# Optimization experiments

Hardware: AMD Instinct MI355X
Metric: run time of the kernel (lower is better)

Reference implementation:

```python
import jax, jax.numpy as jnp
import numpy as np

B, S, D = 4, 2048, 384
H, KVH, HD = 6, 2, 64
GROUPS = H // KVH  # 3
ROPE_THETA = 100000.0


def _rope_tables(seq_len, head_dim, theta):
    inv = 1.0 / (theta ** (np.arange(0, head_dim, 2, dtype=np.float32) / head_dim))
    t = np.arange(seq_len, dtype=np.float32)
    freqs = np.outer(t, inv)  # [S, HD//2]
    return jnp.asarray(np.cos(freqs)), jnp.asarray(np.sin(freqs))


def setup_inputs() -> dict:
    key = jax.random.key(0)
    ks = jax.random.split(key, 5)
    hidden_states = jax.random.normal(ks[0], (B, S, D), dtype=jnp.float32)
    Wq = jax.random.normal(ks[1], (D, H * HD), dtype=jnp.float32) * 0.02
    Wk = jax.random.normal(ks[2], (D, KVH * HD), dtype=jnp.float32) * 0.02
    Wv = jax.random.normal(ks[3], (D, KVH * HD), dtype=jnp.float32) * 0.02
    Wo = jax.random.normal(ks[4], (H * HD, D), dtype=jnp.float32) * 0.02
    freqs_cos, freqs_sin = _rope_tables(S, HD, ROPE_THETA)
    return {"hidden_states": hidden_states, "Wq": Wq, "Wk": Wk, "Wv": Wv,
            "Wo": Wo, "freqs_cos": freqs_cos, "freqs_sin": freqs_sin}


def _apply_rope(x, cos, sin):
    # x: [B, S, h, HD]; treat pairs (even, odd) as complex, multiply by e^{i theta}
    xr = x.reshape(*x.shape[:-1], HD // 2, 2)
    x0, x1 = xr[..., 0], xr[..., 1]
    c = cos[None, :, None, :]  # [1, S, 1, HD//2]
    s = sin[None, :, None, :]
    o0 = x0 * c - x1 * s
    o1 = x0 * s + x1 * c
    return jnp.stack([o0, o1], axis=-1).reshape(x.shape)


def reference(hidden_states, Wq, Wk, Wv, Wo, freqs_cos, freqs_sin):
    Bc, Sc, _ = hidden_states.shape
    q = (hidden_states @ Wq).reshape(Bc, Sc, H, HD)
    k = (hidden_states @ Wk).reshape(Bc, Sc, KVH, HD)
    v = (hidden_states @ Wv).reshape(Bc, Sc, KVH, HD)
    q = _apply_rope(q, freqs_cos, freqs_sin)
    k = _apply_rope(k, freqs_cos, freqs_sin)
    # repeat_interleave over the head dim (GQA group broadcast)
    k = jnp.repeat(k, GROUPS, axis=2)  # [B, S, H, HD]
    v = jnp.repeat(v, GROUPS, axis=2)
    scale = 1.0 / jnp.sqrt(jnp.float32(HD))
    scores = jnp.einsum('bqhd,bkhd->bhqk', q, k) * scale  # [B, H, S, S]
    attn = jax.nn.softmax(scores, axis=-1)
    out = jnp.einsum('bhqk,bkhd->bqhd', attn, v)  # [B, S, H, HD]
    out = out.reshape(Bc, Sc, H * HD)
    return out @ Wo
```

## Files before the change

kernel.cpp:

```cpp
#include <hip/hip_runtime.h>
#include <stdint.h>

#define BATCH   4
#define SEQ     2048
#define DMODEL  384
#define NHEAD   6
#define NKVH    2
#define HD      64
#define MTOK    (BATCH*SEQ)
#define NQKV    640
#define QSCALE  0.125f

typedef __bf16 bf16x8 __attribute__((ext_vector_type(8)));
typedef float  f32x16 __attribute__((ext_vector_type(16)));

__device__ inline unsigned short f2bf(float f) {
  union { float f; unsigned int u; } v; v.f = f;
  return (unsigned short)((v.u + 0x7fffu + ((v.u >> 16) & 1u)) >> 16);
}
__device__ inline float bf2f(unsigned short b) {
  union { unsigned int u; float f; } v; v.u = ((unsigned int)b) << 16;
  return v.f;
}
__device__ inline unsigned int pack2bf(float a, float b) {
  return (unsigned int)f2bf(a) | ((unsigned int)f2bf(b) << 16);
}

#define GLOAD16(gsrc, ldst) __builtin_amdgcn_global_load_lds( \
    (const __attribute__((address_space(1))) void*)(gsrc), \
    (__attribute__((address_space(3))) void*)(ldst), 16, 0, 0)

__global__ void prep_kernel(const float* __restrict__ X,
                            const float* __restrict__ Wq, const float* __restrict__ Wk,
                            const float* __restrict__ Wv, const float* __restrict__ Wo,
                            unsigned short* __restrict__ Xb,
                            unsigned short* __restrict__ WT,
                            unsigned short* __restrict__ WoT) {
  int idx = blockIdx.x * 256 + threadIdx.x;
  if (idx < (MTOK*DMODEL)/4) {
    float4 v = ((const float4*)X)[idx];
    union { unsigned short s[4]; uint2 u; } o;
    o.s[0] = f2bf(v.x); o.s[1] = f2bf(v.y); o.s[2] = f2bf(v.z); o.s[3] = f2bf(v.w);
    ((uint2*)Xb)[idx] = o.u;
  } else if (idx < (MTOK*DMODEL)/4 + NQKV*DMODEL) {
    int j = idx - (MTOK*DMODEL)/4;
    int n = j / DMODEL, k = j % DMODEL;
    float val = (n < 384) ? Wq[k*384 + n]
              : (n < 512) ? Wk[k*128 + (n-384)]
                          : Wv[k*128 + (n-512)];
    WT[j] = f2bf(val);
  } else if (idx < (MTOK*DMODEL)/4 + NQKV*DMODEL + DMODEL*DMODEL) {
    int j = idx - (MTOK*DMODEL)/4 - NQKV*DMODEL;
    int n = j / DMODEL, k = j % DMODEL;
    WoT[j] = f2bf(Wo[k*384 + n]);
  }
}

template<int NCOLS, bool OUT_BF16>
__global__ __launch_bounds__(256, 2)
void gemm_kernel(const unsigned short* __restrict__ A,
                 const unsigned short* __restrict__ BT,
                 void* __restrict__ Cout) {
  __shared__ unsigned short ldsA[128*64];
  __shared__ unsigned short ldsB[64*64];
  const int tid = threadIdx.x;
  const int wid = tid >> 6, lane = tid & 63;
  const int g = lane >> 5, l31 = lane & 31;
  const int wm = wid >> 1, wn = wid & 1;
  const int mbase = blockIdx.x * 128, nbase = blockIdx.y * 64;

  f32x16 c[2];
  #pragma unroll
  for (int i = 0; i < 2; ++i)
    #pragma unroll
    for (int r = 0; r < 16; ++r) c[i][r] = 0.f;

  for (int kt = 0; kt < DMODEL; kt += 64) {
    #pragma unroll
    for (int i = 0; i < 4; ++i) {
      int L = ((wid*4 + i) << 10) + lane*16;
      int row = L >> 7;
      int slot = (lane & 7) ^ (row & 7);
      GLOAD16(A + (mbase + row)*DMODEL + kt + slot*8, ((char*)ldsA) + L);
    }
    #pragma unroll
    for (int i = 0; i < 2; ++i) {
      int L = ((wid*2 + i) << 10) + lane*16;
      int row = L >> 7;
      int slot = (lane & 7) ^ (row & 7);
      GLOAD16(BT + (nbase + row)*DMODEL + kt + slot*8, ((char*)ldsB) + L);
    }
    __syncthreads();

    bf16x8 bf[4];
    {
      int row = wn*32 + l31;
      #pragma unroll
      for (int s = 0; s < 4; ++s) {
        int slot = ((s<<1) | g) ^ (row & 7);
        bf[s] = *(const bf16x8*)(((const char*)ldsB) + row*128 + slot*16);
      }
    }
    #pragma unroll
    for (int mt = 0; mt < 2; ++mt) {
      int row = wm*64 + mt*32 + l31;
      #pragma unroll
      for (int s = 0; s < 4; ++s) {
        int slot = ((s<<1) | g) ^ (row & 7);
        bf16x8 af = *(const bf16x8*)(((const char*)ldsA) + row*128 + slot*16);
        c[mt] = __builtin_amdgcn_mfma_f32_32x32x16_bf16(af, bf[s], c[mt], 0, 0, 0);
      }
    }
    __syncthreads();
  }

  #pragma unroll
  for (int mt = 0; mt < 2; ++mt)
    #pragma unroll
    for (int rr = 0; rr < 16; ++rr) {
      int m = mbase + wm*64 + mt*32 + (rr&3) + ((rr>>2)<<3) + (g<<2);
      int n = nbase + wn*32 + l31;
      float val = c[mt][rr];
      if (OUT_BF16) ((unsigned short*)Cout)[m*NCOLS + n] = f2bf(val);
      else          ((float*)Cout)[m*NCOLS + n] = val;
    }
}

__global__ void rope_kernel(unsigned short* __restrict__ qkv,
                            const float* __restrict__ fcos,
                            const float* __restrict__ fsin) {
  int t = blockIdx.x;
  int c = threadIdx.x;
  int s = t & (SEQ-1);
  int i = c & 31, col;
  float scale;
  if (c < 192) { int h = c >> 5;          col = h*64 + 2*i;        scale = QSCALE; }
  else         { int kvh = (c - 192) >> 5; col = 384 + kvh*64 + 2*i; scale = 1.0f; }
  unsigned int w = *(unsigned int*)(qkv + t*NQKV + col);
  float x0 = bf2f((unsigned short)(w & 0xffff));
  float x1 = bf2f((unsigned short)(w >> 16));
  float cs = fcos[s*32 + i], sn = fsin[s*32 + i];
  float o0 = (x0*cs - x1*sn) * scale;
  float o1 = (x0*sn + x1*cs) * scale;
  *(unsigned int*)(qkv + t*NQKV + col) = pack2bf(o0, o1);
}

__global__ void vtrans_kernel(const unsigned short* __restrict__ qkv,
                              unsigned short* __restrict__ VT) {
  int idx = blockIdx.x * 256 + threadIdx.x;
  int sc  = idx & 255;
  int hd  = (idx >> 8) & 63;
  int kvh = (idx >> 14) & 1;
  int b   = idx >> 15;
  union { unsigned short s[8]; uint4 v; } tmp;
  #pragma unroll
  for (int u = 0; u < 8; ++u)
    tmp.s[u] = qkv[(b*SEQ + sc*8 + u)*NQKV + 512 + kvh*64 + hd];
  *(uint4*)(VT + (((b*2 + kvh)*64 + hd) << 11) + sc*8) = tmp.v;
}

__global__ __launch_bounds__(128, 2)
void attn_kernel(const unsigned short* __restrict__ qkv,
                 const unsigned short* __restrict__ VT,
                 unsigned short* __restrict__ attnO) {
  __shared__ unsigned short ldsK[64*64];
  __shared__ unsigned short ldsV[64*64];
  const int tid = threadIdx.x;
  const int wid = tid >> 6, lane = tid & 63;
  const int g = lane >> 5, l31 = lane & 31;
  const int qt = blockIdx.x, b = blockIdx.y, h = blockIdx.z;
  const int kvh = h / 3;
  const int qrow = qt*64 + wid*32 + l31;
  const int token = b*SEQ + qrow;

  bf16x8 qf[4];
  #pragma unroll
  for (int s = 0; s < 4; ++s)
    qf[s] = *(const bf16x8*)(qkv + token*NQKV + h*64 + s*16 + g*8);

  f32x16 acc0, acc1;
  #pragma unroll
  for (int r = 0; r < 16; ++r) { acc0[r] = 0.f; acc1[r] = 0.f; }
  float m = -1e30f, l = 0.f;

  const unsigned short* Kbase = qkv + (b*SEQ)*NQKV + 384 + kvh*64;
  const unsigned short* Vbase = VT + ((b*2 + kvh)*64 << 11);

  for (int kv0 = 0; kv0 < SEQ; kv0 += 64) {
    if (wid == 0) {
      #pragma unroll
      for (int i = 0; i < 8; ++i) {
        int L = (i << 10) + lane*16;
        int row = L >> 7;
        int slot = (lane & 7) ^ (row & 7);
        GLOAD16(Kbase + (kv0 + row)*NQKV + slot*8, ((char*)ldsK) + L);
      }
    } else {
      #pragma unroll
      for (int i = 0; i < 8; ++i) {
        int L = (i << 10) + lane*16;
        int row = L >> 7;
        int slot = (lane & 7) ^ (row & 7);
        GLOAD16(Vbase + (row << 11) + kv0 + slot*8, ((char*)ldsV) + L);
      }
    }
    __syncthreads();

    f32x16 c1[2];
    #pragma unroll
    for (int kvt = 0; kvt < 2; ++kvt) {
      f32x16 cc;
      #pragma unroll
      for (int r = 0; r < 16; ++r) cc[r] = 0.f;
      int row = kvt*32 + l31;
      #pragma unroll
      for (int s = 0; s < 4; ++s) {
        int slot = ((s<<1) | g) ^ (row & 7);
        bf16x8 kf = *(const bf16x8*)(((const char*)ldsK) + row*128 + slot*16);
        cc = __builtin_amdgcn_mfma_f32_32x32x16_bf16(kf, qf[s], cc, 0, 0, 0);
      }
      c1[kvt] = cc;
    }

    float pmax = -1e30f;
    #pragma unroll
    for (int kvt = 0; kvt < 2; ++kvt)
      #pragma unroll
      for (int r = 0; r < 16; ++r) pmax = fmaxf(pmax, c1[kvt][r]);
    pmax = fmaxf(pmax, __shfl_xor(pmax, 32));
    float mnew = fmaxf(m, pmax);
    float alpha = __expf(m - mnew);
    float psum = 0.f;
    #pragma unroll
    for (int kvt = 0; kvt < 2; ++kvt)
      #pragma unroll
      for (int r = 0; r < 16; ++r) {
        float p = __expf(c1[kvt][r] - mnew);
        c1[kvt][r] = p;
        psum += p;
      }
    psum += __shfl_xor(psum, 32);
    l = l*alpha + psum;
    m = mnew;
    #pragma unroll
    for (int r = 0; r < 16; ++r) { acc0[r] *= alpha; acc1[r] *= alpha; }

    #pragma unroll
    for (int kvt = 0; kvt < 2; ++kvt) {
      #pragma unroll
      for (int sl = 0; sl < 2; ++sl) {
        int rbase = sl*8;
        unsigned int w0  = pack2bf(c1[kvt][rbase+0], c1[kvt][rbase+1]);
        unsigned int w1  = pack2bf(c1[kvt][rbase+2], c1[kvt][rbase+3]);
        unsigned int wh0 = pack2bf(c1[kvt][rbase+4], c1[kvt][rbase+5]);
        unsigned int wh1 = pack2bf(c1[kvt][rbase+6], c1[kvt][rbase+7]);
        unsigned int sx0  = __shfl_xor(w0, 32);
        unsigned int sx1  = __shfl_xor(w1, 32);
        unsigned int sxh0 = __shfl_xor(wh0, 32);
        unsigned int sxh1 = __shfl_xor(wh1, 32);
        union { bf16x8 v; unsigned int u[4]; } pf;
        pf.u[0] = g ? sxh0 : w0;
        pf.u[1] = g ? sxh1 : w1;
        pf.u[2] = g ? wh0  : sx0;
        pf.u[3] = g ? wh1  : sx1;
        int kvslice = kvt*32 + sl*16;
        #pragma unroll
        for (int dt = 0; dt < 2; ++dt) {
          int row = dt*32 + l31;
          int slot = ((kvslice >> 3) + g) ^ (row & 7);
          bf16x8 vf = *(const bf16x8*)(((const char*)ldsV) + row*128 + slot*16);
          if (dt == 0) acc0 = __builtin_amdgcn_mfma_f32_32x32x16_bf16(vf, pf.v, acc0, 0, 0, 0);
          else         acc1 = __builtin_amdgcn_mfma_f32_32x32x16_bf16(vf, pf.v, acc1, 0, 0, 0);
        }
      }
    }
    __syncthreads();
  }

  float invl = 1.0f / l;
  #pragma unroll
  for (int dt = 0; dt < 2; ++dt)
    #pragma unroll
    for (int q8 = 0; q8 < 4; ++q8) {
      union { unsigned short s[4]; uint2 u; } ov;
      #pragma unroll
      for (int j = 0; j < 4; ++j) {
        float v = (dt ? acc1[q8*4+j] : acc0[q8*4+j]) * invl;
        ov.s[j] = f2bf(v);
      }
      int d = dt*32 + q8*8 + g*4;
      *(uint2*)(attnO + token*DMODEL + h*64 + d) = ov.u;
    }
}

extern "C" void kernel_launch(void* const* d_in, const int* in_sizes, int n_in,
                              void* d_out, int out_size, void* d_ws, size_t ws_size,
                              hipStream_t stream) {
  const float* X    = (const float*)d_in[0];
  const float* Wq   = (const float*)d_in[1];
  const float* Wk   = (const float*)d_in[2];
  const float* Wv   = (const float*)d_in[3];
  const float* Wo   = (const float*)d_in[4];
  const float* fcos = (const float*)d_in[5];
  const float* fsin = (const float*)d_in[6];
  char* ws = (char*)d_ws;

  unsigned short* Xb    = (unsigned short*)(ws);
  unsigned short* QKV   = (unsigned short*)(ws + 6291456);
  unsigned short* VTb   = (unsigned short*)(ws + 16777216);
  unsigned short* attnO = (unsigned short*)(ws + 18874368);
  unsigned short* WT    = (unsigned short*)(ws + 25165824);
  unsigned short* WoT   = (unsigned short*)(ws + 25657344);

  prep_kernel<<<4608, 256, 0, stream>>>(X, Wq, Wk, Wv, Wo, Xb, WT, WoT);
  gemm_kernel<NQKV, true><<<dim3(64, 10), 256, 0, stream>>>(Xb, WT, QKV);
  rope_kernel<<<MTOK, 256, 0, stream>>>(QKV, fcos, fsin);
  vtrans_kernel<<<512, 256, 0, stream>>>(QKV, VTb);
  attn_kernel<<<dim3(32, BATCH, NHEAD), 128, 0, stream>>>(QKV, VTb, attnO);
  gemm_kernel<DMODEL, false><<<dim3(64, 6), 256, 0, stream>>>(attnO, WoT, (void*)d_out);
}
```

Before: 181.5 us.

## Split KV across waves with double-buffered staging, exp2 softmax, LDS V transpose

Restructures attention so each wave handles half of the KV sequence for 32 query rows, double-buffers its own K/V tiles via async global-to-LDS loads with vmcnt waits instead of block barriers, and merges the two partial softmax states at the end through shared memory. It also folds log2(e) into the Q scale to use raw v_exp_f32, skips the rescale when the running max barely grows, packs bf16 with a hardware convert, remaps blocks for L2 locality, and rewrites the V transpose to go through an LDS tile for coalesced access. Together these aim to remove barrier stalls and exposed load latency and to shrink softmax ALU cost. In exchange the grid has more, smaller blocks, there is a cross-wave combine step, and the lazy-rescale threshold allows unnormalized values up to 2^10.

```diff
diff --git a/kernel.cpp b/kernel.cpp
--- a/kernel.cpp
+++ b/kernel.cpp
@@ -9,7 +9,7 @@
 #define HD      64
 #define MTOK    (BATCH*SEQ)
 #define NQKV    640
-#define QSCALE  0.125f
+#define QSCALE  (0.125f * 1.4426950408889634f)
 
 typedef __bf16 bf16x8 __attribute__((ext_vector_type(8)));
 typedef float  f32x16 __attribute__((ext_vector_type(16)));
@@ -25,10 +25,23 @@
 __device__ inline unsigned int pack2bf(float a, float b) {
   return (unsigned int)f2bf(a) | ((unsigned int)f2bf(b) << 16);
 }
+__device__ inline unsigned int cvtpk(float lo, float hi) {
+  unsigned int r;
+  asm("v_cvt_pk_bf16_f32 %0, %1, %2" : "=v"(r) : "v"(lo), "v"(hi));
+  return r;
+}
+__device__ inline float exp2_fast(float x) {
+  float r;
+  asm("v_exp_f32 %0, %1" : "=v"(r) : "v"(x));
+  return r;
+}
 
 #define GLOAD16(gsrc, ldst) __builtin_amdgcn_global_load_lds( \
     (const __attribute__((address_space(1))) void*)(gsrc), \
     (__attribute__((address_space(3))) void*)(ldst), 16, 0, 0)
+
+#define WAITV8() asm volatile("s_waitcnt vmcnt(8)" ::: "memory")
+#define WAITV0() asm volatile("s_waitcnt vmcnt(0)" ::: "memory")
 
 __global__ void prep_kernel(const float* __restrict__ X,
                             const float* __restrict__ Wq, const float* __restrict__ Wk,
@@ -147,150 +160,195 @@
 
 __global__ void vtrans_kernel(const unsigned short* __restrict__ qkv,
                               unsigned short* __restrict__ VT) {
-  int idx = blockIdx.x * 256 + threadIdx.x;
-  int sc  = idx & 255;
-  int hd  = (idx >> 8) & 63;
-  int kvh = (idx >> 14) & 1;
-  int b   = idx >> 15;
-  union { unsigned short s[8]; uint4 v; } tmp;
-  #pragma unroll
-  for (int u = 0; u < 8; ++u)
-    tmp.s[u] = qkv[(b*SEQ + sc*8 + u)*NQKV + 512 + kvh*64 + hd];
-  *(uint4*)(VT + (((b*2 + kvh)*64 + hd) << 11) + sc*8) = tmp.v;
+  __shared__ unsigned short tile[64][72];
+  int t = threadIdx.x;
+  int s0 = blockIdx.x * 64;
+  int kvh = blockIdx.y;
+  int b = blockIdx.z;
+  #pragma unroll
+  for (int p = 0; p < 2; ++p) {
+    int row = (t >> 3) + p*32;
+    int c8 = t & 7;
+    uint4 v = *(const uint4*)(qkv + (size_t)(b*SEQ + s0 + row)*NQKV + 512 + kvh*64 + c8*8);
+    *(uint4*)(&tile[row][c8*8]) = v;
+  }
+  __syncthreads();
+  #pragma unroll
+  for (int p = 0; p < 2; ++p) {
+    int d = (t >> 3) + p*32;
+    int sj = t & 7;
+    union { unsigned short s[8]; uint4 v; } o;
+    #pragma unroll
+    for (int u = 0; u < 8; ++u) o.s[u] = tile[sj*8 + u][d];
+    *(uint4*)(VT + (size_t)((b*2 + kvh)*64 + d)*SEQ + s0 + sj*8) = o.v;
+  }
+}
+
+__device__ __forceinline__ void stage_tile(const unsigned short* Kbase,
+                                           const unsigned short* Vbase,
+                                           int kv0, char* kbuf, char* vbuf, int lane) {
+  #pragma unroll
+  for (int i = 0; i < 4; ++i) {
+    int L = (i << 10) + lane*16;
+    int row = L >> 7;
+    int slot = (lane & 7) ^ (row & 7);
+    GLOAD16(Kbase + (kv0 + row)*NQKV + slot*8, kbuf + L);
+  }
+  #pragma unroll
+  for (int i = 0; i < 4; ++i) {
+    int L = (i << 10) + lane*16;
+    int row = L >> 6;
+    int sl4 = (lane & 3) ^ (row & 3) ^ ((row >> 2) & 3);
+    GLOAD16(Vbase + row*SEQ + kv0 + sl4*8, vbuf + L);
+  }
 }
 
 __global__ __launch_bounds__(128, 2)
 void attn_kernel(const unsigned short* __restrict__ qkv,
                  const unsigned short* __restrict__ VT,
                  unsigned short* __restrict__ attnO) {
-  __shared__ unsigned short ldsK[64*64];
-  __shared__ unsigned short ldsV[64*64];
+  __shared__ __align__(16) char smem[32768];
   const int tid = threadIdx.x;
   const int wid = tid >> 6, lane = tid & 63;
   const int g = lane >> 5, l31 = lane & 31;
-  const int qt = blockIdx.x, b = blockIdx.y, h = blockIdx.z;
+
+  int bid = blockIdx.x;
+  int e = (bid & 7)*192 + (bid >> 3);
+  int qt = e & 63;
+  int hb = e >> 6;
+  int h = hb % 6, b = hb / 6;
   const int kvh = h / 3;
-  const int qrow = qt*64 + wid*32 + l31;
-  const int token = b*SEQ + qrow;
+  const int token = b*SEQ + qt*32 + l31;
+  const int kvbase = wid * (SEQ/2);
+
+  char* kb0 = smem + wid*16384;
+  char* vb0 = kb0 + 4096;
 
   bf16x8 qf[4];
   #pragma unroll
   for (int s = 0; s < 4; ++s)
-    qf[s] = *(const bf16x8*)(qkv + token*NQKV + h*64 + s*16 + g*8);
+    qf[s] = *(const bf16x8*)(qkv + (size_t)token*NQKV + h*64 + s*16 + g*8);
 
   f32x16 acc0, acc1;
   #pragma unroll
   for (int r = 0; r < 16; ++r) { acc0[r] = 0.f; acc1[r] = 0.f; }
   float m = -1e30f, l = 0.f;
 
-  const unsigned short* Kbase = qkv + (b*SEQ)*NQKV + 384 + kvh*64;
-  const unsigned short* Vbase = VT + ((b*2 + kvh)*64 << 11);
-
-  for (int kv0 = 0; kv0 < SEQ; kv0 += 64) {
-    if (wid == 0) {
-      #pragma unroll
-      for (int i = 0; i < 8; ++i) {
-        int L = (i << 10) + lane*16;
-        int row = L >> 7;
-        int slot = (lane & 7) ^ (row & 7);
-        GLOAD16(Kbase + (kv0 + row)*NQKV + slot*8, ((char*)ldsK) + L);
-      }
-    } else {
-      #pragma unroll
-      for (int i = 0; i < 8; ++i) {
-        int L = (i << 10) + lane*16;
-        int row = L >> 7;
-        int slot = (lane & 7) ^ (row & 7);
-        GLOAD16(Vbase + (row << 11) + kv0 + slot*8, ((char*)ldsV) + L);
-      }
-    }
-    __syncthreads();
-
-    f32x16 c1[2];
-    #pragma unroll
-    for (int kvt = 0; kvt < 2; ++kvt) {
-      f32x16 cc;
-      #pragma unroll
-      for (int r = 0; r < 16; ++r) cc[r] = 0.f;
-      int row = kvt*32 + l31;
+  const unsigned short* Kbase = qkv + (size_t)(b*SEQ)*NQKV + 384 + kvh*64;
+  const unsigned short* Vbase = VT + (size_t)((b*2 + kvh)*64)*SEQ;
+
+  stage_tile(Kbase, Vbase, kvbase, kb0, vb0, lane);
+
+  for (int t = 0; t < 32; ++t) {
+    int cur = t & 1;
+    if (t < 31)
+      stage_tile(Kbase, Vbase, kvbase + (t+1)*32,
+                 kb0 + ((t+1)&1)*8192, vb0 + ((t+1)&1)*8192, lane);
+    if (t < 31) { WAITV8(); } else { WAITV0(); }
+
+    const char* kb = kb0 + cur*8192;
+    const char* vb = vb0 + cur*8192;
+
+    f32x16 c1;
+    #pragma unroll
+    for (int r = 0; r < 16; ++r) c1[r] = 0.f;
+    {
+      int row = l31;
       #pragma unroll
       for (int s = 0; s < 4; ++s) {
         int slot = ((s<<1) | g) ^ (row & 7);
-        bf16x8 kf = *(const bf16x8*)(((const char*)ldsK) + row*128 + slot*16);
-        cc = __builtin_amdgcn_mfma_f32_32x32x16_bf16(kf, qf[s], cc, 0, 0, 0);
-      }
-      c1[kvt] = cc;
-    }
-
-    float pmax = -1e30f;
-    #pragma unroll
-    for (int kvt = 0; kvt < 2; ++kvt)
-      #pragma unroll
-      for (int r = 0; r < 16; ++r) pmax = fmaxf(pmax, c1[kvt][r]);
+        bf16x8 kf = *(const bf16x8*)(kb + row*128 + slot*16);
+        c1 = __builtin_amdgcn_mfma_f32_32x32x16_bf16(kf, qf[s], c1, 0, 0, 0);
+      }
+    }
+
+    float pmax = c1[0];
+    #pragma unroll
+    for (int r = 1; r < 16; ++r) pmax = fmaxf(pmax, c1[r]);
     pmax = fmaxf(pmax, __shfl_xor(pmax, 32));
-    float mnew = fmaxf(m, pmax);
-    float alpha = __expf(m - mnew);
-    float psum = 0.f;
-    #pragma unroll
-    for (int kvt = 0; kvt < 2; ++kvt)
+    if (!__all(pmax <= m + 10.f)) {
+      float mnew = fmaxf(m, pmax);
+      float alpha = exp2_fast(m - mnew);
+      #pragma unroll
+      for (int r = 0; r < 16; ++r) { acc0[r] *= alpha; acc1[r] *= alpha; }
+      l *= alpha;
+      m = mnew;
+    }
+    float p[16]; float psum = 0.f;
+    #pragma unroll
+    for (int r = 0; r < 16; ++r) {
+      p[r] = exp2_fast(c1[r] - m);
+      psum += p[r];
+    }
+    l += psum;
+
+    #pragma unroll
+    for (int sl = 0; sl < 2; ++sl) {
+      int rb = sl*8;
+      unsigned int w0  = cvtpk(p[rb+0], p[rb+1]);
+      unsigned int w1  = cvtpk(p[rb+2], p[rb+3]);
+      unsigned int wh0 = cvtpk(p[rb+4], p[rb+5]);
+      unsigned int wh1 = cvtpk(p[rb+6], p[rb+7]);
+      unsigned int s0 = g ? w0 : wh0;
+      unsigned int s1 = g ? w1 : wh1;
+      unsigned int r0 = __shfl_xor(s0, 32);
+      unsigned int r1 = __shfl_xor(s1, 32);
+      union { bf16x8 v; unsigned int u[4]; } pf;
+      pf.u[0] = g ? r0  : w0;
+      pf.u[1] = g ? r1  : w1;
+      pf.u[2] = g ? wh0 : r0;
+      pf.u[3] = g ? wh1 : r1;
+      #pragma unroll
+      for (int dt = 0; dt < 2; ++dt) {
+        int row = dt*32 + l31;
+        int t16 = (sl*2 + g) ^ (row & 3) ^ ((row >> 2) & 3);
+        bf16x8 vf = *(const bf16x8*)(vb + row*64 + t16*16);
+        if (dt == 0) acc0 = __builtin_amdgcn_mfma_f32_32x32x16_bf16(vf, pf.v, acc0, 0, 0, 0);
+        else         acc1 = __builtin_amdgcn_mfma_f32_32x32x16_bf16(vf, pf.v, acc1, 0, 0, 0);
+      }
+    }
+  }
+
+  l += __shfl_xor(l, 32);
+  __syncthreads();
+  float* cmb  = (float*)smem;
+  float* accx = (float*)(smem + 512);
+  if (g == 0) { cmb[wid*64 + l31] = m; cmb[wid*64 + 32 + l31] = l; }
+  __syncthreads();
+  int ow = wid ^ 1;
+  float m_o = cmb[ow*64 + l31], l_o = cmb[ow*64 + 32 + l31];
+  float ms = fmaxf(m, m_o);
+  float a = exp2_fast(m - ms);
+  if (wid == 1) {
+    #pragma unroll
+    for (int dt = 0; dt < 2; ++dt)
       #pragma unroll
       for (int r = 0; r < 16; ++r) {
-        float p = __expf(c1[kvt][r] - mnew);
-        c1[kvt][r] = p;
-        psum += p;
-      }
-    psum += __shfl_xor(psum, 32);
-    l = l*alpha + psum;
-    m = mnew;
-    #pragma unroll
-    for (int r = 0; r < 16; ++r) { acc0[r] *= alpha; acc1[r] *= alpha; }
-
-    #pragma unroll
-    for (int kvt = 0; kvt < 2; ++kvt) {
-      #pragma unroll
-      for (int sl = 0; sl < 2; ++sl) {
-        int rbase = sl*8;
-        unsigned int w0  = pack2bf(c1[kvt][rbase+0], c1[kvt][rbase+1]);
-        unsigned int w1  = pack2bf(c1[kvt][rbase+2], c1[kvt][rbase+3]);
-        unsigned int wh0 = pack2bf(c1[kvt][rbase+4], c1[kvt][rbase+5]);
-        unsigned int wh1 = pack2bf(c1[kvt][rbase+6], c1[kvt][rbase+7]);
-        unsigned int sx0  = __shfl_xor(w0, 32);
-        unsigned int sx1  = __shfl_xor(w1, 32);
-        unsigned int sxh0 = __shfl_xor(wh0, 32);
-        unsigned int sxh1 = __shfl_xor(wh1, 32);
-        union { bf16x8 v; unsigned int u[4]; } pf;
-        pf.u[0] = g ? sxh0 : w0;
-        pf.u[1] = g ? sxh1 : w1;
-        pf.u[2] = g ? wh0  : sx0;
-        pf.u[3] = g ? wh1  : sx1;
-        int kvslice = kvt*32 + sl*16;
+        int d = dt*32 + (r&3) + ((r>>2)<<3) + (g<<2);
+        accx[d*32 + l31] = (dt ? acc1[r] : acc0[r]) * a;
+      }
+  }
+  __syncthreads();
+  if (wid == 0) {
+    float a_o = exp2_fast(m_o - ms);
+    float lstar = l*a + l_o*a_o;
+    float invl = 1.0f / lstar;
+    #pragma unroll
+    for (int dt = 0; dt < 2; ++dt)
+      #pragma unroll
+      for (int q8 = 0; q8 < 4; ++q8) {
+        union { unsigned short s[4]; uint2 u; } ov;
         #pragma unroll
-        for (int dt = 0; dt < 2; ++dt) {
-          int row = dt*32 + l31;
-          int slot = ((kvslice >> 3) + g) ^ (row & 7);
-          bf16x8 vf = *(const bf16x8*)(((const char*)ldsV) + row*128 + slot*16);
-          if (dt == 0) acc0 = __builtin_amdgcn_mfma_f32_32x32x16_bf16(vf, pf.v, acc0, 0, 0, 0);
-          else         acc1 = __builtin_amdgcn_mfma_f32_32x32x16_bf16(vf, pf.v, acc1, 0, 0, 0);
+        for (int j = 0; j < 4; ++j) {
+          int r = q8*4 + j;
+          int d = dt*32 + (r&3) + ((r>>2)<<3) + (g<<2);
+          float tot = (dt ? acc1[r] : acc0[r])*a + accx[d*32 + l31];
+          ov.s[j] = f2bf(tot * invl);
         }
-      }
-    }
-    __syncthreads();
-  }
-
-  float invl = 1.0f / l;
-  #pragma unroll
-  for (int dt = 0; dt < 2; ++dt)
-    #pragma unroll
-    for (int q8 = 0; q8 < 4; ++q8) {
-      union { unsigned short s[4]; uint2 u; } ov;
-      #pragma unroll
-      for (int j = 0; j < 4; ++j) {
-        float v = (dt ? acc1[q8*4+j] : acc0[q8*4+j]) * invl;
-        ov.s[j] = f2bf(v);
-      }
-      int d = dt*32 + q8*8 + g*4;
-      *(uint2*)(attnO + token*DMODEL + h*64 + d) = ov.u;
-    }
+        int d0 = dt*32 + q8*8 + g*4;
+        *(uint2*)(attnO + (size_t)token*DMODEL + h*64 + d0) = ov.u;
+      }
+  }
 }
 
 extern "C" void kernel_launch(void* const* d_in, const int* in_sizes, int n_in,
@@ -315,7 +373,7 @@
   prep_kernel<<<4608, 256, 0, stream>>>(X, Wq, Wk, Wv, Wo, Xb, WT, WoT);
   gemm_kernel<NQKV, true><<<dim3(64, 10), 256, 0, stream>>>(Xb, WT, QKV);
   rope_kernel<<<MTOK, 256, 0, stream>>>(QKV, fcos, fsin);
-  vtrans_kernel<<<512, 256, 0, stream>>>(QKV, VTb);
-  attn_kernel<<<dim3(32, BATCH, NHEAD), 128, 0, stream>>>(QKV, VTb, attnO);
+  vtrans_kernel<<<dim3(32, 2, 4), 256, 0, stream>>>(QKV, VTb);
+  attn_kernel<<<1536, 128, 0, stream>>>(QKV, VTb, attnO);
   gemm_kernel<DMODEL, false><<<dim3(64, 6), 256, 0, stream>>>(attnO, WoT, (void*)d_out);
 }
```

After: 177.4 us. 2.3% less time.
